# Kernel optimization log

Hardware: AMD Instinct MI355X
Metric: run time of the kernel (lower is better)

## Reference

```python
import jax, jax.numpy as jnp
import numpy as np

NF, NV = 400000, 200000
C_IN, C_OUT, K, MULT = 64, 128, 27, 1
BN_EPS = 1e-5


def setup_inputs() -> dict:
    key = jax.random.key(0)
    ks = jax.random.split(key, 8)
    inputs = jax.random.normal(ks[0], (NF, C_IN), dtype=jnp.float32)
    filt_coeff = jax.random.uniform(ks[1], (NF, K), dtype=jnp.float32)
    face = jax.random.randint(ks[2], (NF, 3), 0, NV, dtype=jnp.int32)
    nf_count = jnp.ones((NV,), dtype=jnp.int32)
    vt_map = jnp.arange(NV, dtype=jnp.int64)
    # learned parameters (xavier-ish scale)
    spatial_weights = jax.random.normal(ks[3], (K, C_IN, MULT), dtype=jnp.float32) * np.sqrt(2.0 / (K * C_IN + MULT))
    depth_weights = jax.random.normal(ks[4], (C_IN * MULT, C_OUT), dtype=jnp.float32) * np.sqrt(2.0 / (C_IN * MULT + C_OUT))
    biases = jnp.zeros((1, C_OUT), dtype=jnp.float32)
    gamma = jnp.ones((C_OUT,), dtype=jnp.float32)
    beta = jnp.zeros((C_OUT,), dtype=jnp.float32)
    return {
        "inputs": inputs, "filt_coeff": filt_coeff, "face": face,
        "nf_count": nf_count, "vt_map": vt_map,
        "spatial_weights": spatial_weights, "depth_weights": depth_weights,
        "biases": biases, "gamma": gamma, "beta": beta,
    }


def reference(inputs, filt_coeff, face, nf_count, vt_map,
              spatial_weights, depth_weights, biases, gamma, beta):
    nv = nf_count.shape[0]
    nf = inputs.shape[0]
    # per-face mixture of spatial filters: [Nf, C_in, mult]
    w = jnp.einsum('fk,kcm->fcm', filt_coeff, spatial_weights)
    # per-face weighted features, flattened depthwise: [Nf, C_in*mult]
    contrib = (inputs[:, :, None] * w).reshape(nf, -1)
    # scatter each face's contribution to its 3 vertices
    idx = face.reshape(-1)                                  # [3*Nf]
    vals = jnp.broadcast_to(contrib[:, None, :], (nf, 3, contrib.shape[1])).reshape(3 * nf, -1)
    agg = jax.ops.segment_sum(vals, idx, num_segments=nv)    # [Nv, C_in*mult]
    # average by number of adjacent faces
    denom = jnp.maximum(nf_count, 1).astype(agg.dtype)[:, None]
    agg = agg / denom
    # reorder vertices per vt_map
    agg = agg[vt_map]
    # pointwise (depth) conv + bias + ReLU
    out = agg @ depth_weights + biases
    out = jax.nn.relu(out)
    # BatchNorm1d (training-mode batch statistics over vertices)
    mean = out.mean(axis=0)
    var = out.var(axis=0)
    out = (out - mean) * jax.lax.rsqrt(var + BN_EPS) * gamma + beta
    return out
```

## Files before the change

### kernel.cpp

```cpp
#include <hip/hip_runtime.h>
#include <hip/hip_bf16.h>

#define NFACE 400000
#define NVERT 200000
#define CIN 64
#define COUT 128
#define KF 27
#define BN_EPS 1e-5f
#define LST 56
#define BST 40

typedef __attribute__((ext_vector_type(8))) short bf16x8;
typedef __attribute__((ext_vector_type(4))) float f32x4;

__device__ __forceinline__ short f2bf(float x) {
    __hip_bfloat16 h = __float2bfloat16(x);
    return *reinterpret_cast<short*>(&h);
}
__device__ __forceinline__ float bf2f(unsigned short u) {
    union { unsigned int i; float f; } x; x.i = ((unsigned)u) << 16; return x.f;
}

__global__ __launch_bounds__(256) void prep_k(const float* __restrict__ sw,
                                              const float* __restrict__ dw,
                                              short* __restrict__ swb,
                                              short* __restrict__ dwb) {
    int t = threadIdx.x;
#pragma unroll
    for (int j = 0; j < 10; ++j) {
        int cell = t + j * 256;
        if (cell < 64 * BST) {
            int ch = cell / BST, k = cell % BST;
            float v = (k < KF) ? sw[k * 64 + ch] : 0.f;
            swb[cell] = f2bf(v);
        }
    }
#pragma unroll
    for (int p4 = 0; p4 < 4; ++p4) {
        int p = t + p4 * 256;
        int frag = p >> 6, lane = p & 63;
        int nb = frag >> 3, tt = (frag >> 1) & 3, kk = frag & 1;
        int col = nb * 64 + tt * 16 + (lane & 15);
#pragma unroll
        for (int j = 0; j < 8; ++j) {
            int k = kk * 32 + (lane >> 4) * 8 + j;
            dwb[(size_t)p * 8 + j] = f2bf(dw[k * 128 + col]);
        }
    }
}

__global__ __launch_bounds__(256) void mix_k(
    const float* __restrict__ inputs,
    const float* __restrict__ filt,
    const int*   __restrict__ face,
    const short* __restrict__ swb,
    __hip_bfloat16* __restrict__ contrib,
    int* __restrict__ adj,
    int* __restrict__ adj2)
{
    __shared__ __align__(16) char smem[16384];
    short* Af = (short*)smem;
    short* Bs = (short*)(smem + 7168);
    float (*Wt)[64] = (float (*)[64])smem;

    const int t  = threadIdx.x;
    const int fb = blockIdx.x * 64;

    if (t < 192) {
        int fl = t / 3, vi = t - fl * 3;
        int v = face[(size_t)(fb + fl) * 3 + vi];
        int s = atomicAdd(&adj[(size_t)v * 16], 1);
        if (s < 15)       adj[(size_t)v * 16 + 1 + s] = fb + fl;
        else if (s < 31)  adj2[(size_t)v * 16 + (s - 15)] = fb + fl;
    }

    for (int i = t; i < 320; i += 256)
        ((float4*)Bs)[i] = ((const float4*)swb)[i];
#pragma unroll
    for (int j = 0; j < 4; ++j) {
        int idx = t + j * 256;
        int fl = idx >> 4, k = (idx & 15) * 2;
        const float* fr = filt + (size_t)(fb + fl) * KF;
        float v0 = (k     < KF) ? fr[k]     : 0.f;
        float v1 = (k + 1 < KF) ? fr[k + 1] : 0.f;
        Af[fl * LST + k]     = f2bf(v0);
        Af[fl * LST + k + 1] = f2bf(v1);
    }
    __syncthreads();

    const int lane = t & 63;
    const int wid  = t >> 6;
    const int r0   = wid * 16;

    bf16x8 a = *(const bf16x8*)&Af[(r0 + (lane & 15)) * LST + (lane >> 4) * 8];
    f32x4 acc[4];
#pragma unroll
    for (int cb = 0; cb < 4; ++cb) {
        bf16x8 b = *(const bf16x8*)&Bs[(cb * 16 + (lane & 15)) * BST + (lane >> 4) * 8];
        acc[cb] = __builtin_amdgcn_mfma_f32_16x16x32_bf16(a, b, (f32x4){0.f, 0.f, 0.f, 0.f}, 0, 0, 0);
    }
    __syncthreads();

#pragma unroll
    for (int cb = 0; cb < 4; ++cb)
#pragma unroll
        for (int i = 0; i < 4; ++i)
            Wt[r0 + (lane >> 4) * 4 + i][cb * 16 + (lane & 15)] = acc[cb][i];
    __syncthreads();

#pragma unroll
    for (int p = 0; p < 4; ++p) {
        int idx = (p * 256 + t) * 4;
        int fl = idx >> 6, c = idx & 63;
        float4 in4 = *(const float4*)&inputs[(size_t)(fb + fl) * 64 + c];
        float4 w4  = *(const float4*)&Wt[fl][c];
        short4 o;
        o.x = f2bf(in4.x * w4.x);
        o.y = f2bf(in4.y * w4.y);
        o.z = f2bf(in4.z * w4.z);
        o.w = f2bf(in4.w * w4.w);
        *(short4*)((short*)contrib + (size_t)fb * 64 + idx) = o;
    }
}

#define BV 32
__global__ __launch_bounds__(256) void pconv_k(
    const __hip_bfloat16* __restrict__ contrib,
    const int* __restrict__ adj,
    const int* __restrict__ adj2,
    const int* __restrict__ nf_count,
    const int* __restrict__ vt_map,
    const short* __restrict__ dwb,
    const float* __restrict__ bias,
    __hip_bfloat16* __restrict__ outb,
    float* __restrict__ stats)
{
    __shared__ int   srcL[BV];
    __shared__ float denL[BV];
    __shared__ int   adjL[BV][16];
    __shared__ __align__(16) short A[BV * 64];
    __shared__ __align__(16) short outL[BV * 128];

    const int t     = threadIdx.x;
    const int lane  = t & 63;
    const int wid   = t >> 6;
    const int vbase = blockIdx.x * BV;

    if (t < BV) {
        int src = vt_map[vbase + t];
        srcL[t] = src;
        denL[t] = 1.f / (float)max(nf_count[src], 1);
    }
    __syncthreads();
#pragma unroll
    for (int r = 0; r < 2; ++r) {
        int i = t + r * 256;
        int row = i >> 4, j = i & 15;
        adjL[row][j] = adj[(size_t)srcL[row] * 16 + j];
    }
    __syncthreads();

    for (int q0 = 0; q0 < 8; ++q0) {
        int q = wid * 8 + q0;
        int n = adjL[q][0];
        n = n > 31 ? 31 : n;
        int nm = n > 15 ? 15 : n;
        float acc = 0.f;
        int j = 0;
        for (; j + 4 <= nm; j += 4) {
            int f0 = adjL[q][1 + j + 0];
            int f1 = adjL[q][1 + j + 1];
            int f2 = adjL[q][1 + j + 2];
            int f3 = adjL[q][1 + j + 3];
            float a0 = __bfloat162float(contrib[(size_t)f0 * 64 + lane]);
            float a1 = __bfloat162float(contrib[(size_t)f1 * 64 + lane]);
            float a2 = __bfloat162float(contrib[(size_t)f2 * 64 + lane]);
            float a3 = __bfloat162float(contrib[(size_t)f3 * 64 + lane]);
            acc += (a0 + a1) + (a2 + a3);
        }
        for (; j < nm; ++j) {
            int f = adjL[q][1 + j];
            acc += __bfloat162float(contrib[(size_t)f * 64 + lane]);
        }
        if (n > 15) {
            for (int j2 = 0; j2 < n - 15; ++j2) {
                int f = adj2[(size_t)srcL[q] * 16 + j2];
                acc += __bfloat162float(contrib[(size_t)f * 64 + lane]);
            }
        }
        acc *= denL[q];
        int swz = (lane & 7) | ((((lane >> 3) ^ (q & 7))) << 3);
        A[q * 64 + swz] = f2bf(acc);
    }
    __syncthreads();

    const int mi = wid & 1;
    const int nb = wid >> 1;
    f32x4 acc[4];
#pragma unroll
    for (int tt = 0; tt < 4; ++tt) acc[tt] = (f32x4){0.f, 0.f, 0.f, 0.f};
#pragma unroll
    for (int kk = 0; kk < 2; ++kk) {
        int row = mi * 16 + (lane & 15);
        int chunk = (kk * 4 + (lane >> 4)) ^ (row & 7);
        bf16x8 a = *(const bf16x8*)&A[row * 64 + chunk * 8];
#pragma unroll
        for (int tt = 0; tt < 4; ++tt) {
            int frag = (nb * 4 + tt) * 2 + kk;
            bf16x8 b = *(const bf16x8*)&dwb[((size_t)frag * 64 + lane) * 8];
            acc[tt] = __builtin_amdgcn_mfma_f32_16x16x32_bf16(a, b, acc[tt], 0, 0, 0);
        }
    }

    float* st = stats + (blockIdx.x & 7) * 256;
#pragma unroll
    for (int tt = 0; tt < 4; ++tt) {
        int col = nb * 64 + tt * 16 + (lane & 15);
        float bv = bias[col];
        float s = 0.f, s2 = 0.f;
#pragma unroll
        for (int i = 0; i < 4; ++i) {
            float o = fmaxf(acc[tt][i] + bv, 0.f);
            int row = mi * 16 + (lane >> 4) * 4 + i;
            outL[row * 128 + col] = f2bf(o);
            s  += o;
            s2 += o * o;
        }
        s  += __shfl_xor(s, 16);  s  += __shfl_xor(s, 32);
        s2 += __shfl_xor(s2, 16); s2 += __shfl_xor(s2, 32);
        if ((lane >> 4) == 0) {
            atomicAdd(&st[col], s);
            atomicAdd(&st[128 + col], s2);
        }
    }
    __syncthreads();

#pragma unroll
    for (int r = 0; r < 2; ++r) {
        int i = t + r * 256;
        ((int4*)&outb[(size_t)vbase * 128])[i] = ((const int4*)outL)[i];
    }
}

__global__ __launch_bounds__(256) void bn_k(
    const __hip_bfloat16* __restrict__ outb,
    float* __restrict__ out,
    const float* __restrict__ stats,
    const float* __restrict__ gamma,
    const float* __restrict__ beta)
{
    __shared__ float sc[128], sh[128];
    if (threadIdx.x < 128) {
        int c = threadIdx.x;
        float s = 0.f, s2 = 0.f;
#pragma unroll
        for (int r = 0; r < 8; ++r) {
            s  += stats[r * 256 + c];
            s2 += stats[r * 256 + 128 + c];
        }
        float mean = s / (float)NVERT;
        float var  = s2 / (float)NVERT - mean * mean;
        float inv  = rsqrtf(var + BN_EPS) * gamma[c];
        sc[c] = inv;
        sh[c] = beta[c] - mean * inv;
    }
    __syncthreads();

    const unsigned short* ob = (const unsigned short*)outb;
    float4* o4 = (float4*)out;
    size_t total4 = (size_t)NVERT * COUT / 4;
    for (size_t i = (size_t)blockIdx.x * 256 + threadIdx.x; i < total4;
         i += (size_t)gridDim.x * 256) {
        int c0 = (int)((i * 4) & 127);
        ushort4 u = *(const ushort4*)&ob[i * 4];
        float4 v;
        v.x = bf2f(u.x) * sc[c0 + 0] + sh[c0 + 0];
        v.y = bf2f(u.y) * sc[c0 + 1] + sh[c0 + 1];
        v.z = bf2f(u.z) * sc[c0 + 2] + sh[c0 + 2];
        v.w = bf2f(u.w) * sc[c0 + 3] + sh[c0 + 3];
        o4[i] = v;
    }
}

extern "C" void kernel_launch(void* const* d_in, const int* in_sizes, int n_in,
                              void* d_out, int out_size, void* d_ws, size_t ws_size,
                              hipStream_t stream) {
    const float* inputs   = (const float*)d_in[0];
    const float* filt     = (const float*)d_in[1];
    const int*   face     = (const int*)d_in[2];
    const int*   nf_count = (const int*)d_in[3];
    const int*   vt_map   = (const int*)d_in[4];
    const float* sw       = (const float*)d_in[5];
    const float* dw       = (const float*)d_in[6];
    const float* bias     = (const float*)d_in[7];
    const float* gamma    = (const float*)d_in[8];
    const float* beta     = (const float*)d_in[9];
    float* out = (float*)d_out;

    float*          stats = (float*)d_ws;
    short*          swb   = (short*)((char*)d_ws + 8192);
    short*          dwb   = (short*)((char*)d_ws + 16384);
    __hip_bfloat16* outb  = (__hip_bfloat16*)((char*)d_ws + 32768);

    __hip_bfloat16* contrib = (__hip_bfloat16*)d_out;
    int* adj  = (int*)((char*)d_out + (size_t)NFACE * CIN * 2);
    int* adj2 = (int*)((char*)adj + (size_t)NVERT * 16 * 4);

    hipMemsetAsync(stats, 0, 8192, stream);
    hipMemsetAsync(adj, 0, (size_t)NVERT * 16 * sizeof(int), stream);

    prep_k<<<1, 256, 0, stream>>>(sw, dw, swb, dwb);
    mix_k<<<NFACE / 64, 256, 0, stream>>>(inputs, filt, face, swb,
                                          contrib, adj, adj2);
    pconv_k<<<NVERT / BV, 256, 0, stream>>>(contrib, adj, adj2, nf_count,
                                            vt_map, dwb, bias, outb, stats);
    bn_k<<<2048, 256, 0, stream>>>(outb, out, stats, gamma, beta);
}
```

Measured before the change: 232.3 us.

## Replicate per-vertex adjacency buckets across copies with a global overflow list

Face-to-vertex adjacency is now spread over 8 replicated 8-int buckets, chosen by block index, to lower atomic contention on per-vertex counters. Faces past 7 per copy go to a global overflow list. The point-conv kernel gathers all copies, flattens them into a shared list per vertex, and scans the overflow list. The cost is four times more memset and adjacency read traffic, a serial flatten step, and a lower cap on faces per vertex.

```diff
diff --git a/kernel.cpp b/kernel.cpp
--- a/kernel.cpp
+++ b/kernel.cpp
@@ -9,6 +9,8 @@
 #define BN_EPS 1e-5f
 #define LST 56
 #define BST 40
+#define NCPY 8
+#define OVF_CAP 4096
 
 typedef __attribute__((ext_vector_type(8))) short bf16x8;
 typedef __attribute__((ext_vector_type(4))) float f32x4;
@@ -55,8 +57,9 @@
     const int*   __restrict__ face,
     const short* __restrict__ swb,
     __hip_bfloat16* __restrict__ contrib,
-    int* __restrict__ adj,
-    int* __restrict__ adj2)
+    int* __restrict__ adjc,
+    int* __restrict__ ovf,
+    int* __restrict__ ovf_cnt)
 {
     __shared__ __align__(16) char smem[16384];
     short* Af = (short*)smem;
@@ -65,13 +68,18 @@
 
     const int t  = threadIdx.x;
     const int fb = blockIdx.x * 64;
+    const int cp = blockIdx.x & (NCPY - 1);
 
     if (t < 192) {
         int fl = t / 3, vi = t - fl * 3;
         int v = face[(size_t)(fb + fl) * 3 + vi];
-        int s = atomicAdd(&adj[(size_t)v * 16], 1);
-        if (s < 15)       adj[(size_t)v * 16 + 1 + s] = fb + fl;
-        else if (s < 31)  adj2[(size_t)v * 16 + (s - 15)] = fb + fl;
+        int* row = adjc + ((size_t)cp * NVERT + v) * 8;
+        int s = atomicAdd(row, 1);
+        if (s < 7) row[1 + s] = fb + fl;
+        else {
+            int pos = atomicAdd(ovf_cnt, 1);
+            if (pos < OVF_CAP) { ovf[pos * 2] = v; ovf[pos * 2 + 1] = fb + fl; }
+        }
     }
 
     for (int i = t; i < 320; i += 256)
@@ -126,8 +134,9 @@
 #define BV 32
 __global__ __launch_bounds__(256) void pconv_k(
     const __hip_bfloat16* __restrict__ contrib,
-    const int* __restrict__ adj,
-    const int* __restrict__ adj2,
+    const int* __restrict__ adjc,
+    const int* __restrict__ ovf,
+    const int* __restrict__ ovf_cnt,
     const int* __restrict__ nf_count,
     const int* __restrict__ vt_map,
     const short* __restrict__ dwb,
@@ -137,7 +146,9 @@
 {
     __shared__ int   srcL[BV];
     __shared__ float denL[BV];
-    __shared__ int   adjL[BV][16];
+    __shared__ int   adjL[NCPY][BV][8];
+    __shared__ int   flatL[BV][26];
+    __shared__ int   fcnt[BV];
     __shared__ __align__(16) short A[BV * 64];
     __shared__ __align__(16) short outL[BV * 128];
 
@@ -153,40 +164,49 @@
     }
     __syncthreads();
 #pragma unroll
-    for (int r = 0; r < 2; ++r) {
+    for (int r = 0; r < 8; ++r) {
         int i = t + r * 256;
-        int row = i >> 4, j = i & 15;
-        adjL[row][j] = adj[(size_t)srcL[row] * 16 + j];
+        int copy = i >> 8, row = (i >> 3) & 31, j = i & 7;
+        adjL[copy][row][j] = adjc[((size_t)copy * NVERT + srcL[row]) * 8 + j];
+    }
+    __syncthreads();
+
+    if (t < BV) {
+        int cnt = 0;
+#pragma unroll
+        for (int copy = 0; copy < NCPY; ++copy) {
+            int n = adjL[copy][t][0];
+            n = n > 7 ? 7 : n;
+            for (int j = 0; j < n; ++j)
+                if (cnt < 26) flatL[t][cnt++] = adjL[copy][t][1 + j];
+        }
+        int oc = *ovf_cnt;
+        oc = oc > OVF_CAP ? OVF_CAP : oc;
+        for (int j = 0; j < oc; ++j)
+            if (ovf[2 * j] == srcL[t] && cnt < 26) flatL[t][cnt++] = ovf[2 * j + 1];
+        fcnt[t] = cnt;
     }
     __syncthreads();
 
     for (int q0 = 0; q0 < 8; ++q0) {
         int q = wid * 8 + q0;
-        int n = adjL[q][0];
-        n = n > 31 ? 31 : n;
-        int nm = n > 15 ? 15 : n;
+        int n = fcnt[q];
         float acc = 0.f;
         int j = 0;
-        for (; j + 4 <= nm; j += 4) {
-            int f0 = adjL[q][1 + j + 0];
-            int f1 = adjL[q][1 + j + 1];
-            int f2 = adjL[q][1 + j + 2];
-            int f3 = adjL[q][1 + j + 3];
+        for (; j + 4 <= n; j += 4) {
+            int f0 = flatL[q][j + 0];
+            int f1 = flatL[q][j + 1];
+            int f2 = flatL[q][j + 2];
+            int f3 = flatL[q][j + 3];
             float a0 = __bfloat162float(contrib[(size_t)f0 * 64 + lane]);
             float a1 = __bfloat162float(contrib[(size_t)f1 * 64 + lane]);
             float a2 = __bfloat162float(contrib[(size_t)f2 * 64 + lane]);
             float a3 = __bfloat162float(contrib[(size_t)f3 * 64 + lane]);
             acc += (a0 + a1) + (a2 + a3);
         }
-        for (; j < nm; ++j) {
-            int f = adjL[q][1 + j];
+        for (; j < n; ++j) {
+            int f = flatL[q][j];
             acc += __bfloat162float(contrib[(size_t)f * 64 + lane]);
-        }
-        if (n > 15) {
-            for (int j2 = 0; j2 < n - 15; ++j2) {
-                int f = adj2[(size_t)srcL[q] * 16 + j2];
-                acc += __bfloat162float(contrib[(size_t)f * 64 + lane]);
-            }
         }
         acc *= denL[q];
         int swz = (lane & 7) | ((((lane >> 3) ^ (q & 7))) << 3);
@@ -297,22 +317,25 @@
     const float* beta     = (const float*)d_in[9];
     float* out = (float*)d_out;
 
-    float*          stats = (float*)d_ws;
-    short*          swb   = (short*)((char*)d_ws + 8192);
-    short*          dwb   = (short*)((char*)d_ws + 16384);
-    __hip_bfloat16* outb  = (__hip_bfloat16*)((char*)d_ws + 32768);
+    char* w = (char*)d_ws;
+    float*          stats  = (float*)w;
+    int*            ovfcnt = (int*)(w + 8192);
+    int*            ovf    = (int*)(w + 8192 + 64);
+    short*          swb    = (short*)(w + 8192 + 64 + OVF_CAP * 8);
+    short*          dwb    = (short*)(w + 8192 + 64 + OVF_CAP * 8 + 5120);
+    __hip_bfloat16* outb   = (__hip_bfloat16*)(w + 8192 + 64 + OVF_CAP * 8 + 5120 + 16384);
 
     __hip_bfloat16* contrib = (__hip_bfloat16*)d_out;
-    int* adj  = (int*)((char*)d_out + (size_t)NFACE * CIN * 2);
-    int* adj2 = (int*)((char*)adj + (size_t)NVERT * 16 * 4);
-
-    hipMemsetAsync(stats, 0, 8192, stream);
-    hipMemsetAsync(adj, 0, (size_t)NVERT * 16 * sizeof(int), stream);
+    int* adjc = (int*)((char*)d_out + (size_t)NFACE * CIN * 2);
+
+    hipMemsetAsync(d_ws, 0, 8192 + 64, stream);
+    hipMemsetAsync(adjc, 0, (size_t)NCPY * NVERT * 8 * 4, stream);
 
     prep_k<<<1, 256, 0, stream>>>(sw, dw, swb, dwb);
     mix_k<<<NFACE / 64, 256, 0, stream>>>(inputs, filt, face, swb,
-                                          contrib, adj, adj2);
-    pconv_k<<<NVERT / BV, 256, 0, stream>>>(contrib, adj, adj2, nf_count,
-                                            vt_map, dwb, bias, outb, stats);
+                                          contrib, adjc, ovf, ovfcnt);
+    pconv_k<<<NVERT / BV, 256, 0, stream>>>(contrib, adjc, ovf, ovfcnt,
+                                            nf_count, vt_map, dwb, bias,
+                                            outb, stats);
     bn_k<<<2048, 256, 0, stream>>>(outb, out, stats, gamma, beta);
 }
```

Result: slower. 258.5 us (+11.3%).

## Build vertex-to-face CSR via bucketed counting sort instead of atomic adjacency slots

Applied to the files above, without the earlier changes.

Replaces the per-vertex atomic slot adjacency lists built inside mix_k with a multi-pass counting sort (histogram, scan, scatter into 512-vertex buckets, per-bucket CSR build). pconv_k then reads contiguous CSR rows via row offsets instead of the padded 16-int adjacency slots and the overflow array. It removes the adjacency memset and the scattered global atomics, but adds four extra launches, a single-block serial scan over 256 block counts, and extra traffic for the intermediate pair array. The gather step is also capped at 32 faces per vertex.

```diff
diff --git a/kernel.cpp b/kernel.cpp
--- a/kernel.cpp
+++ b/kernel.cpp
@@ -10,6 +10,11 @@
 #define LST 56
 #define BST 40
 
+#define M_TOT (NFACE * 3)
+#define NB    391
+#define NBLK  256
+#define CHUNK ((M_TOT + NBLK - 1) / NBLK)
+
 typedef __attribute__((ext_vector_type(8))) short bf16x8;
 typedef __attribute__((ext_vector_type(4))) float f32x4;
 
@@ -49,14 +54,118 @@
     }
 }
 
+__global__ __launch_bounds__(256) void hist_k(const int* __restrict__ faceflat,
+                                              int* __restrict__ blockcnt) {
+    __shared__ int h[512];
+    const int t = threadIdx.x, blk = blockIdx.x;
+    for (int j = t; j < 512; j += 256) h[j] = 0;
+    __syncthreads();
+    int e0 = blk * CHUNK;
+    int e1 = min(e0 + CHUNK, M_TOT);
+    for (int e = e0 + t; e < e1; e += 256)
+        atomicAdd(&h[faceflat[e] >> 9], 1);
+    __syncthreads();
+    for (int j = t; j < 512; j += 256) blockcnt[blk * 512 + j] = h[j];
+}
+
+__global__ __launch_bounds__(256) void scan_k(int* __restrict__ blockcnt,
+                                              int* __restrict__ bucket_start,
+                                              int* __restrict__ row_off) {
+    __shared__ int tot[512];
+    __shared__ int bst[512];
+    const int t = threadIdx.x;
+    for (int b = t; b < 512; b += 256) {
+        int acc = 0;
+        if (b < NB)
+            for (int k = 0; k < NBLK; ++k) acc += blockcnt[k * 512 + b];
+        tot[b] = acc;
+    }
+    __syncthreads();
+    if (t < 64) {
+        int base8 = t * 8, loc[8], s = 0;
+#pragma unroll
+        for (int j = 0; j < 8; ++j) { loc[j] = s; s += tot[base8 + j]; }
+        int v = s;
+        for (int off = 1; off < 64; off <<= 1) {
+            int u = __shfl_up(v, off);
+            if (t >= off) v += u;
+        }
+        int excl = v - s;
+#pragma unroll
+        for (int j = 0; j < 8; ++j) bst[base8 + j] = excl + loc[j];
+    }
+    __syncthreads();
+    for (int b = t; b < NB; b += 256) bucket_start[b] = bst[b];
+    if (t == 0) { bucket_start[NB] = bst[NB]; row_off[NVERT] = M_TOT; }
+    for (int b = t; b < NB; b += 256) {
+        int acc = bst[b];
+        for (int k = 0; k < NBLK; ++k) {
+            int c = blockcnt[k * 512 + b];
+            blockcnt[k * 512 + b] = acc;
+            acc += c;
+        }
+    }
+}
+
+__global__ __launch_bounds__(256) void scat_k(const int* __restrict__ faceflat,
+                                              const int* __restrict__ blockcnt,
+                                              int2* __restrict__ pairs) {
+    __shared__ int baseL[512];
+    __shared__ int lc[512];
+    const int t = threadIdx.x, blk = blockIdx.x;
+    for (int j = t; j < 512; j += 256) { baseL[j] = blockcnt[blk * 512 + j]; lc[j] = 0; }
+    __syncthreads();
+    int e0 = blk * CHUNK;
+    int e1 = min(e0 + CHUNK, M_TOT);
+    for (int e = e0 + t; e < e1; e += 256) {
+        int v = faceflat[e];
+        int b = v >> 9;
+        int l = atomicAdd(&lc[b], 1);
+        pairs[baseL[b] + l] = make_int2(v, e / 3);
+    }
+}
+
+__global__ __launch_bounds__(256) void csr_k(const int2* __restrict__ pairs,
+                                             const int* __restrict__ bucket_start,
+                                             int* __restrict__ row_off,
+                                             int* __restrict__ csr) {
+    __shared__ int cnt[512], esc[512], pc[512];
+    const int t = threadIdx.x, b = blockIdx.x;
+    const int p0 = bucket_start[b], p1 = bucket_start[b + 1];
+    const int vbase = b << 9;
+    for (int j = t; j < 512; j += 256) { cnt[j] = 0; pc[j] = 0; }
+    __syncthreads();
+    for (int i = p0 + t; i < p1; i += 256)
+        atomicAdd(&cnt[pairs[i].x - vbase], 1);
+    __syncthreads();
+    if (t < 64) {
+        int base8 = t * 8, loc[8], s = 0;
+#pragma unroll
+        for (int j = 0; j < 8; ++j) { loc[j] = s; s += cnt[base8 + j]; }
+        int v = s;
+        for (int off = 1; off < 64; off <<= 1) {
+            int u = __shfl_up(v, off);
+            if (t >= off) v += u;
+        }
+        int excl = v - s;
+#pragma unroll
+        for (int j = 0; j < 8; ++j) esc[base8 + j] = excl + loc[j];
+    }
+    __syncthreads();
+    int nvb = min(512, NVERT - vbase);
+    for (int j = t; j < nvb; j += 256) row_off[vbase + j] = p0 + esc[j];
+    for (int i = p0 + t; i < p1; i += 256) {
+        int lv = pairs[i].x - vbase;
+        int l = atomicAdd(&pc[lv], 1);
+        csr[p0 + esc[lv] + l] = pairs[i].y;
+    }
+}
+
 __global__ __launch_bounds__(256) void mix_k(
     const float* __restrict__ inputs,
     const float* __restrict__ filt,
-    const int*   __restrict__ face,
     const short* __restrict__ swb,
-    __hip_bfloat16* __restrict__ contrib,
-    int* __restrict__ adj,
-    int* __restrict__ adj2)
+    __hip_bfloat16* __restrict__ contrib)
 {
     __shared__ __align__(16) char smem[16384];
     short* Af = (short*)smem;
@@ -65,14 +174,6 @@
 
     const int t  = threadIdx.x;
     const int fb = blockIdx.x * 64;
-
-    if (t < 192) {
-        int fl = t / 3, vi = t - fl * 3;
-        int v = face[(size_t)(fb + fl) * 3 + vi];
-        int s = atomicAdd(&adj[(size_t)v * 16], 1);
-        if (s < 15)       adj[(size_t)v * 16 + 1 + s] = fb + fl;
-        else if (s < 31)  adj2[(size_t)v * 16 + (s - 15)] = fb + fl;
-    }
 
     for (int i = t; i < 320; i += 256)
         ((float4*)Bs)[i] = ((const float4*)swb)[i];
@@ -126,8 +227,8 @@
 #define BV 32
 __global__ __launch_bounds__(256) void pconv_k(
     const __hip_bfloat16* __restrict__ contrib,
-    const int* __restrict__ adj,
-    const int* __restrict__ adj2,
+    const int* __restrict__ row_off,
+    const int* __restrict__ csr,
     const int* __restrict__ nf_count,
     const int* __restrict__ vt_map,
     const short* __restrict__ dwb,
@@ -135,9 +236,10 @@
     __hip_bfloat16* __restrict__ outb,
     float* __restrict__ stats)
 {
-    __shared__ int   srcL[BV];
     __shared__ float denL[BV];
-    __shared__ int   adjL[BV][16];
+    __shared__ int   offL[BV];
+    __shared__ int   degL[BV];
+    __shared__ int   flatL[BV][32];
     __shared__ __align__(16) short A[BV * 64];
     __shared__ __align__(16) short outL[BV * 128];
 
@@ -148,45 +250,40 @@
 
     if (t < BV) {
         int src = vt_map[vbase + t];
-        srcL[t] = src;
         denL[t] = 1.f / (float)max(nf_count[src], 1);
-    }
-    __syncthreads();
-#pragma unroll
-    for (int r = 0; r < 2; ++r) {
+        int o = row_off[src];
+        int d = row_off[src + 1] - o;
+        offL[t] = o;
+        degL[t] = d > 32 ? 32 : d;
+    }
+    __syncthreads();
+#pragma unroll
+    for (int r = 0; r < 4; ++r) {
         int i = t + r * 256;
-        int row = i >> 4, j = i & 15;
-        adjL[row][j] = adj[(size_t)srcL[row] * 16 + j];
+        int row = i >> 5, j = i & 31;
+        if (j < degL[row]) flatL[row][j] = csr[offL[row] + j];
     }
     __syncthreads();
 
     for (int q0 = 0; q0 < 8; ++q0) {
         int q = wid * 8 + q0;
-        int n = adjL[q][0];
-        n = n > 31 ? 31 : n;
-        int nm = n > 15 ? 15 : n;
+        int n = degL[q];
         float acc = 0.f;
         int j = 0;
-        for (; j + 4 <= nm; j += 4) {
-            int f0 = adjL[q][1 + j + 0];
-            int f1 = adjL[q][1 + j + 1];
-            int f2 = adjL[q][1 + j + 2];
-            int f3 = adjL[q][1 + j + 3];
+        for (; j + 4 <= n; j += 4) {
+            int f0 = flatL[q][j + 0];
+            int f1 = flatL[q][j + 1];
+            int f2 = flatL[q][j + 2];
+            int f3 = flatL[q][j + 3];
             float a0 = __bfloat162float(contrib[(size_t)f0 * 64 + lane]);
             float a1 = __bfloat162float(contrib[(size_t)f1 * 64 + lane]);
             float a2 = __bfloat162float(contrib[(size_t)f2 * 64 + lane]);
             float a3 = __bfloat162float(contrib[(size_t)f3 * 64 + lane]);
             acc += (a0 + a1) + (a2 + a3);
         }
-        for (; j < nm; ++j) {
-            int f = adjL[q][1 + j];
+        for (; j < n; ++j) {
+            int f = flatL[q][j];
             acc += __bfloat162float(contrib[(size_t)f * 64 + lane]);
-        }
-        if (n > 15) {
-            for (int j2 = 0; j2 < n - 15; ++j2) {
-                int f = adj2[(size_t)srcL[q] * 16 + j2];
-                acc += __bfloat162float(contrib[(size_t)f * 64 + lane]);
-            }
         }
         acc *= denL[q];
         int swz = (lane & 7) | ((((lane >> 3) ^ (q & 7))) << 3);
@@ -297,22 +394,30 @@
     const float* beta     = (const float*)d_in[9];
     float* out = (float*)d_out;
 
-    float*          stats = (float*)d_ws;
-    short*          swb   = (short*)((char*)d_ws + 8192);
-    short*          dwb   = (short*)((char*)d_ws + 16384);
-    __hip_bfloat16* outb  = (__hip_bfloat16*)((char*)d_ws + 32768);
-
-    __hip_bfloat16* contrib = (__hip_bfloat16*)d_out;
-    int* adj  = (int*)((char*)d_out + (size_t)NFACE * CIN * 2);
-    int* adj2 = (int*)((char*)adj + (size_t)NVERT * 16 * 4);
+    char* w = (char*)d_ws;
+    float*          stats = (float*)w;
+    short*          swb   = (short*)(w + 8192);
+    short*          dwb   = (short*)(w + 16384);
+    __hip_bfloat16* outb  = (__hip_bfloat16*)(w + 32768);
+
+    char* o = (char*)d_out;
+    __hip_bfloat16* contrib      = (__hip_bfloat16*)o;
+    int2*           pairs        = (int2*)(o + 51200000);
+    int*            csr          = (int*)(o + 60800000);
+    int*            row_off      = (int*)(o + 65600000);
+    int*            blockcnt     = (int*)(o + 66400256);
+    int*            bucket_start = (int*)(o + 66924544);
+    const int*      faceflat     = face;
 
     hipMemsetAsync(stats, 0, 8192, stream);
-    hipMemsetAsync(adj, 0, (size_t)NVERT * 16 * sizeof(int), stream);
 
     prep_k<<<1, 256, 0, stream>>>(sw, dw, swb, dwb);
-    mix_k<<<NFACE / 64, 256, 0, stream>>>(inputs, filt, face, swb,
-                                          contrib, adj, adj2);
-    pconv_k<<<NVERT / BV, 256, 0, stream>>>(contrib, adj, adj2, nf_count,
+    hist_k<<<NBLK, 256, 0, stream>>>(faceflat, blockcnt);
+    scan_k<<<1, 256, 0, stream>>>(blockcnt, bucket_start, row_off);
+    scat_k<<<NBLK, 256, 0, stream>>>(faceflat, blockcnt, pairs);
+    csr_k<<<NB, 256, 0, stream>>>(pairs, bucket_start, row_off, csr);
+    mix_k<<<NFACE / 64, 256, 0, stream>>>(inputs, filt, swb, contrib);
+    pconv_k<<<NVERT / BV, 256, 0, stream>>>(contrib, row_off, csr, nf_count,
                                             vt_map, dwb, bias, outb, stats);
     bn_k<<<2048, 256, 0, stream>>>(outb, out, stats, gamma, beta);
 }
```

New measurement: 230.3 us. No clear change (-0.9%).
